# Performance work log

Hardware: AMD Instinct MI355X
Metric: run time of the kernel (lower is better)

The kernel has to match this reference:

```python
import jax, jax.numpy as jnp
import numpy as np

B, S, HID = 1, 2048, 2048
H, HKV, D = 16, 4, 128
GROUPS = H // HKV
SCALE = D ** -0.5


def rotate_half(x):
    x1, x2 = x[..., : x.shape[-1] // 2], x[..., x.shape[-1] // 2 :]
    return jnp.concatenate((-x2, x1), axis=-1)


def setup_inputs() -> dict:
    key = jax.random.key(0)
    ks = jax.random.split(key, 8)
    hidden_states = jax.random.normal(ks[0], (B, S, HID), dtype=jnp.float32)
    # standard RoPE tables, base 10000
    inv_freq = 1.0 / (10000.0 ** (np.arange(0, D, 2, dtype=np.float32) / D))
    t = np.arange(S, dtype=np.float32)
    freqs = np.outer(t, inv_freq)                      # (S, D/2)
    emb = np.concatenate([freqs, freqs], axis=-1)      # (S, D)
    cos = jnp.asarray(np.cos(emb)[None], dtype=jnp.float32)  # (1, S, D)
    sin = jnp.asarray(np.sin(emb)[None], dtype=jnp.float32)
    std = 0.02
    Wq = jax.random.normal(ks[1], (HID, H * D), dtype=jnp.float32) * std
    Wk = jax.random.normal(ks[2], (HID, HKV * D), dtype=jnp.float32) * std
    Wv = jax.random.normal(ks[3], (HID, HKV * D), dtype=jnp.float32) * std
    Wg = jax.random.normal(ks[4], (HID, HKV), dtype=jnp.float32) * std
    Wo = jax.random.normal(ks[5], (H * D, HID), dtype=jnp.float32) * std
    return {"hidden_states": hidden_states, "cos": cos, "sin": sin,
            "Wq": Wq, "Wk": Wk, "Wv": Wv, "Wg": Wg, "Wo": Wo}


def reference(hidden_states, cos, sin, Wq, Wk, Wv, Wg, Wo):
    b, s, _ = hidden_states.shape
    # projections -> (B, heads, S, D)
    q = (hidden_states @ Wq).reshape(b, s, H, D).transpose(0, 2, 1, 3)
    k = (hidden_states @ Wk).reshape(b, s, HKV, D).transpose(0, 2, 1, 3)
    v = (hidden_states @ Wv).reshape(b, s, HKV, D).transpose(0, 2, 1, 3)
    g = (hidden_states @ Wg).transpose(0, 2, 1)                 # (B, HKV, S)
    g = jax.nn.log_sigmoid(g.astype(jnp.float32))
    # RoPE
    c, sn = cos[:, None, :, :], sin[:, None, :, :]
    q = q * c + rotate_half(q) * sn
    k = k * c + rotate_half(k) * sn
    # GQA repeat kv heads
    k = jnp.repeat(k, GROUPS, axis=1)
    v = jnp.repeat(v, GROUPS, axis=1)
    g = jnp.repeat(g, GROUPS, axis=1)                           # (B, H, S)
    # gated power retention, deg=2, parallel (quadratic) form
    G = jnp.cumsum(g, axis=-1)                                  # (B, H, S)
    # decay_ij = exp(G_i - G_j) for j <= i  (<= 1 since logsigmoid < 0)
    logdecay = G[..., :, None] - G[..., None, :]                # (B, H, S, S)
    causal = jnp.tril(jnp.ones((s, s), dtype=bool))
    decay = jnp.where(causal, jnp.exp(logdecay), 0.0)
    qk = jnp.einsum("bhid,bhjd->bhij", q, k) * SCALE
    scores = (qk * qk) * decay                                  # deg=2 power scores
    den = jnp.maximum(jnp.sum(scores, axis=-1, keepdims=True), 1.0)
    out = jnp.einsum("bhij,bhjd->bhid", scores, v) / den        # (B, H, S, D)
    out = out.transpose(0, 2, 1, 3).reshape(b, s, H * D)
    return out @ Wo
```

## Files before the change

kernel.cpp:

```cpp
#include <hip/hip_runtime.h>
#include <hip/hip_bf16.h>

#define S_LEN 2048
#define HID   2048
#define NH    16
#define NKV   4
#define HD    128
#define KVD   512
#define NQKV  3072
#define SCALE2 0.0078125f
#define NCH   80

typedef __bf16 bf16;
typedef __attribute__((ext_vector_type(8))) __bf16 bf16x8;
typedef __attribute__((ext_vector_type(4))) float f32x4;

__device__ __forceinline__ void gload_lds16(const bf16* g, bf16* l) {
    __builtin_amdgcn_global_load_lds((const __attribute__((address_space(1))) void*)g,
                                     (__attribute__((address_space(3))) void*)l, 16, 0, 0);
}

__device__ __forceinline__ void transpose_tile(const float* __restrict__ W,
                                               bf16* __restrict__ Wt,
                                               int K, int N, int bx, int by,
                                               int t, float (*Ts)[65])
{
    const int kb = bx * 64, nb = by * 64;
    const int tr = t >> 6, tc = t & 63;
    #pragma unroll
    for (int p = 0; p < 16; ++p) {
        int k = p * 4 + tr;
        Ts[k][tc] = W[(size_t)(kb + k) * N + nb + tc];
    }
    __syncthreads();
    const int nr = t >> 3, kc = t & 7;
    #pragma unroll
    for (int p = 0; p < 2; ++p) {
        int n = p * 32 + nr;
        bf16x8 o;
        #pragma unroll
        for (int x = 0; x < 8; ++x) o[x] = (bf16)Ts[kc * 8 + x][n];
        *(bf16x8*)&Wt[(size_t)(nb + n) * K + kb + kc * 8] = o;
    }
}

__global__ __launch_bounds__(256) void prep_kernel(const float* __restrict__ hs,
                                                   const float* __restrict__ Wq,
                                                   const float* __restrict__ Wk,
                                                   const float* __restrict__ Wv,
                                                   const float* __restrict__ Wo,
                                                   const float* __restrict__ Wg,
                                                   bf16* __restrict__ hsb,
                                                   bf16* __restrict__ WcatT,
                                                   bf16* __restrict__ WoT,
                                                   float* __restrict__ graw,
                                                   float* __restrict__ outz)
{
    __shared__ float Ts[64][65];
    const int b = blockIdx.x, tid = threadIdx.x;

    if (b < 2048) {
        int i = (b * 256 + tid) * 8;
        const float4* qp = (const float4*)&hs[i];
        float4 a = qp[0], c = qp[1];
        bf16x8 r;
        r[0]=(bf16)a.x; r[1]=(bf16)a.y; r[2]=(bf16)a.z; r[3]=(bf16)a.w;
        r[4]=(bf16)c.x; r[5]=(bf16)c.y; r[6]=(bf16)c.z; r[7]=(bf16)c.w;
        *(bf16x8*)&hsb[i] = r;
    } else if (b < 3072) {
        int lb = b - 2048;
        transpose_tile(Wq, WcatT, HID, HID, lb >> 5, lb & 31, tid, Ts);
    } else if (b < 3328) {
        int lb = b - 3072;
        transpose_tile(Wk, WcatT + (size_t)2048 * HID, HID, KVD, lb >> 3, lb & 7, tid, Ts);
    } else if (b < 3584) {
        int lb = b - 3328;
        transpose_tile(Wv, WcatT + (size_t)2560 * HID, HID, KVD, lb >> 3, lb & 7, tid, Ts);
    } else if (b < 4608) {
        int lb = b - 3584;
        transpose_tile(Wo, WoT, HID, HID, lb >> 5, lb & 31, tid, Ts);
    } else if (b < 6656) {
        int i = ((b - 4608) * 256 + tid) * 8;
        float4 z = make_float4(0.f, 0.f, 0.f, 0.f);
        *(float4*)&outz[i] = z;
        *(float4*)&outz[i + 4] = z;
    } else {
        const int w = tid >> 6, lane = tid & 63;
        const int s = (b - 6656) * 4 + w;
        float a0 = 0.f, a1 = 0.f, a2 = 0.f, a3 = 0.f;
        for (int kk = lane; kk < HID; kk += 64) {
            float h = hs[(size_t)s * HID + kk];
            const float* wr = &Wg[kk * 4];
            a0 += h * wr[0]; a1 += h * wr[1];
            a2 += h * wr[2]; a3 += h * wr[3];
        }
        #pragma unroll
        for (int off = 32; off >= 1; off >>= 1) {
            a0 += __shfl_xor(a0, off); a1 += __shfl_xor(a1, off);
            a2 += __shfl_xor(a2, off); a3 += __shfl_xor(a3, off);
        }
        if (lane == 0) {
            float vv[4] = {a0, a1, a2, a3};
            #pragma unroll
            for (int c = 0; c < 4; ++c) {
                float x = vv[c];
                graw[c * S_LEN + s] = fminf(x, 0.f) - log1pf(expf(-fabsf(x)));
            }
        }
    }
}

__device__ __forceinline__ void gemm128_core(const bf16* __restrict__ A,
                                             const bf16* __restrict__ Bt,
                                             int K, int k0, int k1, int mb, int nb,
                                             bf16 (*As)[32], bf16 (*Bs)[32],
                                             f32x4 (*acc)[4],
                                             int w, int l16, int quad, int lane)
{
    const int m0 = (w & 1) * 64, n0 = (w >> 1) * 64;
    const int srow = lane >> 2, scol = (lane & 3) * 8;

    for (int kt = k0; kt < k1; kt += 32) {
        __syncthreads();
        gload_lds16(&A [(size_t)(mb + w * 32 +      srow) * K + kt + scol], &As[w * 32     ][0]);
        gload_lds16(&A [(size_t)(mb + w * 32 + 16 + srow) * K + kt + scol], &As[w * 32 + 16][0]);
        gload_lds16(&Bt[(size_t)(nb + w * 32 +      srow) * K + kt + scol], &Bs[w * 32     ][0]);
        gload_lds16(&Bt[(size_t)(nb + w * 32 + 16 + srow) * K + kt + scol], &Bs[w * 32 + 16][0]);
        __syncthreads();

        bf16x8 af[4], bfr[4];
        #pragma unroll
        for (int t = 0; t < 4; ++t) af[t]  = *(const bf16x8*)&As[m0 + t * 16 + l16][quad * 8];
        #pragma unroll
        for (int u = 0; u < 4; ++u) bfr[u] = *(const bf16x8*)&Bs[n0 + u * 16 + l16][quad * 8];
        #pragma unroll
        for (int t = 0; t < 4; ++t)
            #pragma unroll
            for (int u = 0; u < 4; ++u)
                acc[t][u] = __builtin_amdgcn_mfma_f32_16x16x32_bf16(af[t], bfr[u], acc[t][u], 0, 0, 0);
    }
}

__global__ __launch_bounds__(256) void gemm_qkv_kernel(const bf16* __restrict__ A,
                                                       const bf16* __restrict__ Wt,
                                                       float* __restrict__ qsl,
                                                       float* __restrict__ ksl,
                                                       float* __restrict__ vsl,
                                                       int M, int K)
{
    __shared__ __attribute__((aligned(16))) bf16 As[128][32];
    __shared__ __attribute__((aligned(16))) bf16 Bs[128][32];
    const int tid = threadIdx.x, w = tid >> 6, lane = tid & 63;
    const int l16 = lane & 15, quad = lane >> 4;
    const int mb = blockIdx.x * 128, nb = blockIdx.y * 128;
    const int m0 = (w & 1) * 64, n0 = (w >> 1) * 64;
    const int z = blockIdx.z, kh = K >> 1, k0 = z * kh;

    float* qd = qsl + (size_t)z * S_LEN * HID;
    float* kd = ksl + (size_t)z * S_LEN * KVD;
    float* vd = vsl + (size_t)z * S_LEN * KVD;

    f32x4 acc[4][4] = {};
    gemm128_core(A, Wt, K, k0, k0 + kh, mb, nb, As, Bs, acc, w, l16, quad, lane);

    #pragma unroll
    for (int t = 0; t < 4; ++t)
        #pragma unroll
        for (int u = 0; u < 4; ++u)
            #pragma unroll
            for (int r = 0; r < 4; ++r) {
                int row = mb + m0 + t * 16 + quad * 4 + r;
                int col = nb + n0 + u * 16 + l16;
                float val = acc[t][u][r];
                if (nb < 2048)       qd[(size_t)row * HID + col] = val;
                else if (nb < 2560)  kd[(size_t)row * KVD + (col - 2048)] = val;
                else                 vd[(size_t)(col - 2560) * S_LEN + row] = val;
            }
}

__global__ __launch_bounds__(256) void gemm_wo_kernel(const bf16* __restrict__ A,
                                                      const bf16* __restrict__ Bt,
                                                      float* __restrict__ C,
                                                      int M, int N, int K)
{
    __shared__ __attribute__((aligned(16))) bf16 As[128][32];
    __shared__ __attribute__((aligned(16))) bf16 Bs[128][32];
    const int tid = threadIdx.x, w = tid >> 6, lane = tid & 63;
    const int l16 = lane & 15, quad = lane >> 4;
    const int mb = blockIdx.x * 128, nb = blockIdx.y * 128;
    const int m0 = (w & 1) * 64, n0 = (w >> 1) * 64;
    const int kh = K >> 1, k0 = blockIdx.z * kh;

    f32x4 acc[4][4] = {};
    gemm128_core(A, Bt, K, k0, k0 + kh, mb, nb, As, Bs, acc, w, l16, quad, lane);

    #pragma unroll
    for (int t = 0; t < 4; ++t)
        #pragma unroll
        for (int u = 0; u < 4; ++u)
            #pragma unroll
            for (int r = 0; r < 4; ++r) {
                int row = mb + m0 + t * 16 + quad * 4 + r;
                int col = nb + n0 + u * 16 + l16;
                unsafeAtomicAdd(&C[(size_t)row * N + col], acc[t][u][r]);
            }
}

#define RQB (S_LEN * NH * 64 / 256)
#define RKB (S_LEN * NKV * 64 / 256)
#define RVB (S_LEN * KVD / 8 / 256)
__global__ __launch_bounds__(256) void rope_kernel(const float* __restrict__ qsl,
                                                   const float* __restrict__ ksl,
                                                   const float* __restrict__ vsl,
                                                   bf16* __restrict__ qb,
                                                   bf16* __restrict__ kb,
                                                   bf16* __restrict__ vT,
                                                   const float* __restrict__ cosb,
                                                   const float* __restrict__ sinb,
                                                   const float* __restrict__ graw,
                                                   float* __restrict__ G)
{
    const int blk = blockIdx.x;
    if (blk < RQB + RKB) {
        int idx = blk * 256 + threadIdx.x;
        const float* src; size_t ssz; bf16* dst; int s, rem, stride;
        if (blk < RQB) {
            src = qsl; ssz = (size_t)S_LEN * HID; dst = qb; stride = HID;
            s = idx / (NH * 64); rem = idx % (NH * 64);
        } else {
            idx -= RQB * 256;
            src = ksl; ssz = (size_t)S_LEN * KVD; dst = kb; stride = KVD;
            s = idx / (NKV * 64); rem = idx % (NKV * 64);
        }
        int h = rem >> 6, d = rem & 63;
        size_t base = (size_t)s * stride + h * 128 + d;
        float x0 = src[base]      + src[ssz + base];
        float x1 = src[base + 64] + src[ssz + base + 64];
        float c0 = cosb[s * 128 + d], c1 = cosb[s * 128 + d + 64];
        float n0 = sinb[s * 128 + d], n1 = sinb[s * 128 + d + 64];
        dst[base]      = (bf16)(x0 * c0 - x1 * n0);
        dst[base + 64] = (bf16)(x1 * c1 + x0 * n1);
    } else if (blk < RQB + RKB + RVB) {
        int i = ((blk - RQB - RKB) * 256 + threadIdx.x) * 8;
        const size_t ssz = (size_t)S_LEN * KVD;
        bf16x8 r;
        #pragma unroll
        for (int x = 0; x < 8; ++x) r[x] = (bf16)(vsl[i + x] + vsl[ssz + i + x]);
        *(bf16x8*)&vT[i] = r;
    } else {
        const int c = blk - (RQB + RKB + RVB);
        const int t = threadIdx.x;
        __shared__ float sums[256];
        float loc[8];
        float run = 0.f;
        #pragma unroll
        for (int i = 0; i < 8; ++i) { run += graw[c * S_LEN + t * 8 + i]; loc[i] = run; }
        sums[t] = run;
        __syncthreads();
        for (int off = 1; off < 256; off <<= 1) {
            float add = (t >= off) ? sums[t - off] : 0.f;
            __syncthreads();
            sums[t] += add;
            __syncthreads();
        }
        float offset = sums[t] - run;
        #pragma unroll
        for (int i = 0; i < 8; ++i) G[c * S_LEN + t * 8 + i] = offset + loc[i];
    }
}

__global__ __launch_bounds__(256) void attn_kernel(const bf16* __restrict__ q,
                                                   const bf16* __restrict__ k,
                                                   const bf16* __restrict__ vT,
                                                   const float* __restrict__ G,
                                                   bf16* __restrict__ out,
                                                   float* __restrict__ pO,
                                                   float* __restrict__ pden)
{
    int rem = blockIdx.x, qt = 0, cch = 0;
    #pragma unroll
    for (int g = 0; g < 4; ++g) {
        int sz = 8 * (g + 1);
        if (rem < sz) { qt = g * 8 + rem / (g + 1); cch = rem % (g + 1); break; }
        rem -= sz;
    }
    const int gg = qt >> 3, nc = gg + 1;
    const int jt0 = cch * 8, jt1 = min(qt + 1, jt0 + 8);

    const int h = blockIdx.y, kvh = h >> 2;
    const int qb = qt * 64;
    const int tid = threadIdx.x, w = tid >> 6, lane = tid & 63;
    const int l16 = lane & 15, quad = lane >> 4;

    __shared__ __attribute__((aligned(16))) bf16 Ks4[4][64][32];
    __shared__ __attribute__((aligned(16))) bf16 Vt4[2][128][32];
    __shared__ __attribute__((aligned(16))) bf16 Sb[4][16][68];

    bf16x8 qf[4];
    const int qrow = qb + w * 16 + l16;
    #pragma unroll
    for (int kc = 0; kc < 4; ++kc)
        qf[kc] = *(const bf16x8*)&q[(size_t)qrow * HID + h * HD + kc * 32 + quad * 8];

    const int irow = qb + w * 16 + quad * 4;
    float Gq[4];
    #pragma unroll
    for (int r = 0; r < 4; ++r) Gq[r] = G[kvh * S_LEN + irow + r];

    const int sr4 = lane >> 2, sc4 = (lane & 3) * 8;
    const int vkk = w >> 1, vdg = (w & 1) * 4;

    f32x4 acco[8] = {};
    float den[4] = {0.f, 0.f, 0.f, 0.f};

    for (int kt = jt0; kt < jt1; ++kt) {
        const int jb = kt * 64;
        __syncthreads();
        #pragma unroll
        for (int rg = 0; rg < 4; ++rg)
            gload_lds16(&k[(size_t)(jb + rg * 16 + sr4) * KVD + kvh * HD + w * 32 + sc4],
                        &Ks4[w][rg * 16][0]);
        #pragma unroll
        for (int it = 0; it < 4; ++it)
            gload_lds16(&vT[(size_t)(kvh * HD + (vdg + it) * 16 + sr4) * S_LEN + jb + vkk * 32 + sc4],
                        &Vt4[vkk][(vdg + it) * 16][0]);
        __syncthreads();

        f32x4 accs[4] = {};
        #pragma unroll
        for (int t = 0; t < 4; ++t)
            #pragma unroll
            for (int kc = 0; kc < 4; ++kc) {
                bf16x8 bfr = *(const bf16x8*)&Ks4[kc][t * 16 + l16][quad * 8];
                accs[t] = __builtin_amdgcn_mfma_f32_16x16x32_bf16(qf[kc], bfr, accs[t], 0, 0, 0);
            }

        const float Gt = G[kvh * S_LEN + jb];
        float sr[4];
        #pragma unroll
        for (int r = 0; r < 4; ++r) sr[r] = SCALE2 * __expf(Gq[r] - Gt);
        #pragma unroll
        for (int t = 0; t < 4; ++t) {
            int j = jb + t * 16 + l16;
            float colF = __expf(fminf(Gt - G[kvh * S_LEN + j], 85.f));
            #pragma unroll
            for (int r = 0; r < 4; ++r) {
                float d0 = accs[t][r];
                float sc = (j <= irow + r) ? d0 * d0 * sr[r] * colF : 0.f;
                den[r] += sc;
                Sb[w][quad * 4 + r][t * 16 + l16] = (bf16)sc;
            }
        }

        #pragma unroll
        for (int kk = 0; kk < 2; ++kk) {
            bf16x8 af = *(const bf16x8*)&Sb[w][l16][kk * 32 + quad * 8];
            #pragma unroll
            for (int dt = 0; dt < 8; ++dt) {
                bf16x8 bfr = *(const bf16x8*)&Vt4[kk][dt * 16 + l16][quad * 8];
                acco[dt] = __builtin_amdgcn_mfma_f32_16x16x32_bf16(af, bfr, acco[dt], 0, 0, 0);
            }
        }
    }

    #pragma unroll
    for (int r = 0; r < 4; ++r) {
        #pragma unroll
        for (int off = 1; off < 16; off <<= 1) den[r] += __shfl_xor(den[r], off);
    }

    if (nc == 1) {
        float dinv[4];
        #pragma unroll
        for (int r = 0; r < 4; ++r) dinv[r] = 1.f / fmaxf(den[r], 1.f);
        #pragma unroll
        for (int dt = 0; dt < 8; ++dt)
            #pragma unroll
            for (int r = 0; r < 4; ++r)
                out[(size_t)(irow + r) * HID + h * HD + dt * 16 + l16] =
                    (bf16)(acco[dt][r] * dinv[r]);
    } else {
        const int slot = h * NCH + 4 * gg * (gg + 1) + (qt & 7) * (gg + 1) + cch;
        float* po = &pO[(size_t)slot * 8192];
        const int lr = w * 16 + quad * 4;
        #pragma unroll
        for (int dt = 0; dt < 8; ++dt)
            #pragma unroll
            for (int r = 0; r < 4; ++r)
                po[(lr + r) * 128 + dt * 16 + l16] = acco[dt][r];
        if (l16 == 0) {
            #pragma unroll
            for (int r = 0; r < 4; ++r) pden[slot * 64 + lr + r] = den[r];
        }
    }
}

__global__ __launch_bounds__(256) void attn_reduce_kernel(const float* __restrict__ pO,
                                                          const float* __restrict__ pden,
                                                          bf16* __restrict__ out)
{
    const int p = blockIdx.x;
    const int h = p / 24, qt = 8 + p % 24;
    const int gg = qt >> 3, nc = gg + 1;
    const int base = h * NCH + 4 * gg * (gg + 1) + (qt & 7) * (gg + 1);
    const int qb = qt * 64;
    const int tid = threadIdx.x;

    __shared__ float sden[64];
    if (tid < 64) {
        float s = 0.f;
        for (int c = 0; c < nc; ++c) s += pden[(base + c) * 64 + tid];
        sden[tid] = 1.f / fmaxf(s, 1.f);
    }
    __syncthreads();

    #pragma unroll
    for (int i = 0; i < 8; ++i) {
        int e = i * 1024 + tid * 4;
        float4 s = make_float4(0.f, 0.f, 0.f, 0.f);
        for (int c = 0; c < nc; ++c) {
            float4 v = *(const float4*)&pO[(size_t)(base + c) * 8192 + e];
            s.x += v.x; s.y += v.y; s.z += v.z; s.w += v.w;
        }
        int lr = e >> 7, col = e & 127;
        float di = sden[lr];
        bf16* o = &out[(size_t)(qb + lr) * HID + h * HD + col];
        o[0] = (bf16)(s.x * di); o[1] = (bf16)(s.y * di);
        o[2] = (bf16)(s.z * di); o[3] = (bf16)(s.w * di);
    }
}

extern "C" void kernel_launch(void* const* d_in, const int* in_sizes, int n_in,
                              void* d_out, int out_size, void* d_ws, size_t ws_size,
                              hipStream_t stream)
{
    const float* hs   = (const float*)d_in[0];
    const float* cosb = (const float*)d_in[1];
    const float* sinb = (const float*)d_in[2];
    const float* Wq   = (const float*)d_in[3];
    const float* Wk   = (const float*)d_in[4];
    const float* Wv   = (const float*)d_in[5];
    const float* Wg   = (const float*)d_in[6];
    const float* Wo   = (const float*)d_in[7];
    float* out = (float*)d_out;

    char* p = (char*)d_ws;
    bf16*  qbuf  = (bf16*)p;  p += (size_t)S_LEN * HID * 2;
    bf16*  kbuf  = (bf16*)p;  p += (size_t)S_LEN * KVD * 2;
    bf16*  vT    = (bf16*)p;  p += (size_t)S_LEN * KVD * 2;
    bf16*  abuf  = (bf16*)p;  p += (size_t)S_LEN * HID * 2;
    bf16*  hsb   = (bf16*)p;  p += (size_t)S_LEN * HID * 2;
    bf16*  WcatT = (bf16*)p;  p += (size_t)NQKV * HID * 2;
    bf16*  WoT   = (bf16*)p;  p += (size_t)HID * HID * 2;
    float* graw  = (float*)p; p += (size_t)NKV * S_LEN * 4;
    float* G     = (float*)p; p += (size_t)NKV * S_LEN * 4;
    float* pO    = (float*)p; p += (size_t)NH * NCH * 8192 * 4;
    float* pden  = (float*)p; p += (size_t)NH * NCH * 64 * 4;

    float* qsl = pO;
    float* ksl = pO + (size_t)8 * 1024 * 1024;
    float* vsl = (float*)abuf;

    prep_kernel<<<7168, 256, 0, stream>>>(hs, Wq, Wk, Wv, Wo, Wg,
                                          hsb, WcatT, WoT, graw, out);
    gemm_qkv_kernel<<<dim3(16, 24, 2), 256, 0, stream>>>(hsb, WcatT, qsl, ksl, vsl, S_LEN, HID);
    rope_kernel<<<RQB + RKB + RVB + NKV, 256, 0, stream>>>(qsl, ksl, vsl, qbuf, kbuf, vT,
                                                           cosb, sinb, graw, G);
    attn_kernel<<<dim3(NCH, NH), 256, 0, stream>>>(qbuf, kbuf, vT, G, abuf, pO, pden);
    attn_reduce_kernel<<<NH * 24, 256, 0, stream>>>(pO, pden, abuf);
    gemm_wo_kernel<<<dim3(16, 16, 2), 256, 0, stream>>>(abuf, WoT, out, S_LEN, HID, HID);
}
```

Before: 295.7 us.

## Triple-buffer LDS tiles in projection GEMMs to overlap global loads with MFMA

Replaces the single-buffered GEMM main loop, which synchronized twice per k-tile, with a three-stage LDS ring. Tiles are prefetched two steps ahead via global_load_lds, with explicit vmcnt waits and a single barrier per iteration. The goal is to hide global-memory latency behind MFMA work in the QKV and Wo projections. In exchange, LDS use per block triples, which may reduce occupancy, and the hand-placed waitcnt and barrier ordering must stay correct.

```diff
diff --git a/kernel.cpp b/kernel.cpp
--- a/kernel.cpp
+++ b/kernel.cpp
@@ -110,35 +110,60 @@
     }
 }
 
-__device__ __forceinline__ void gemm128_core(const bf16* __restrict__ A,
+__device__ __forceinline__ void gemm128_pipe(const bf16* __restrict__ A,
                                              const bf16* __restrict__ Bt,
-                                             int K, int k0, int k1, int mb, int nb,
-                                             bf16 (*As)[32], bf16 (*Bs)[32],
+                                             int K, int k0, int nt, int mb, int nb,
+                                             bf16 (*As)[128][32], bf16 (*Bs)[128][32],
                                              f32x4 (*acc)[4],
                                              int w, int l16, int quad, int lane)
 {
     const int m0 = (w & 1) * 64, n0 = (w >> 1) * 64;
     const int srow = lane >> 2, scol = (lane & 3) * 8;
-
-    for (int kt = k0; kt < k1; kt += 32) {
-        __syncthreads();
-        gload_lds16(&A [(size_t)(mb + w * 32 +      srow) * K + kt + scol], &As[w * 32     ][0]);
-        gload_lds16(&A [(size_t)(mb + w * 32 + 16 + srow) * K + kt + scol], &As[w * 32 + 16][0]);
-        gload_lds16(&Bt[(size_t)(nb + w * 32 +      srow) * K + kt + scol], &Bs[w * 32     ][0]);
-        gload_lds16(&Bt[(size_t)(nb + w * 32 + 16 + srow) * K + kt + scol], &Bs[w * 32 + 16][0]);
-        __syncthreads();
-
+    const bf16* a0 = &A [(size_t)(mb + w * 32 +      srow) * K + k0 + scol];
+    const bf16* a1 = &A [(size_t)(mb + w * 32 + 16 + srow) * K + k0 + scol];
+    const bf16* b0 = &Bt[(size_t)(nb + w * 32 +      srow) * K + k0 + scol];
+    const bf16* b1 = &Bt[(size_t)(nb + w * 32 + 16 + srow) * K + k0 + scol];
+
+#define ISSUE_TILE(T, BUF) do {                                         \
+        gload_lds16(a0 + (size_t)(T) * 32, &As[BUF][w * 32     ][0]);   \
+        gload_lds16(a1 + (size_t)(T) * 32, &As[BUF][w * 32 + 16][0]);   \
+        gload_lds16(b0 + (size_t)(T) * 32, &Bs[BUF][w * 32     ][0]);   \
+        gload_lds16(b1 + (size_t)(T) * 32, &Bs[BUF][w * 32 + 16][0]);   \
+    } while (0)
+
+    ISSUE_TILE(0, 0);
+    ISSUE_TILE(1, 1);
+    asm volatile("s_waitcnt vmcnt(4)" ::: "memory");
+    __builtin_amdgcn_s_barrier();
+    __builtin_amdgcn_sched_barrier(0);
+
+    int cb = 0;
+    for (int t = 0; t < nt; ++t) {
         bf16x8 af[4], bfr[4];
         #pragma unroll
-        for (int t = 0; t < 4; ++t) af[t]  = *(const bf16x8*)&As[m0 + t * 16 + l16][quad * 8];
-        #pragma unroll
-        for (int u = 0; u < 4; ++u) bfr[u] = *(const bf16x8*)&Bs[n0 + u * 16 + l16][quad * 8];
-        #pragma unroll
-        for (int t = 0; t < 4; ++t)
+        for (int x = 0; x < 4; ++x) af[x]  = *(const bf16x8*)&As[cb][m0 + x * 16 + l16][quad * 8];
+        #pragma unroll
+        for (int u = 0; u < 4; ++u) bfr[u] = *(const bf16x8*)&Bs[cb][n0 + u * 16 + l16][quad * 8];
+        #pragma unroll
+        for (int x = 0; x < 4; ++x)
             #pragma unroll
             for (int u = 0; u < 4; ++u)
-                acc[t][u] = __builtin_amdgcn_mfma_f32_16x16x32_bf16(af[t], bfr[u], acc[t][u], 0, 0, 0);
-    }
+                acc[x][u] = __builtin_amdgcn_mfma_f32_16x16x32_bf16(af[x], bfr[u], acc[x][u], 0, 0, 0);
+
+        if (t + 2 < nt) {
+            const int ib = (cb == 0) ? 2 : cb - 1;
+            ISSUE_TILE(t + 2, ib);
+            asm volatile("s_waitcnt vmcnt(4)" ::: "memory");
+            __builtin_amdgcn_s_barrier();
+            __builtin_amdgcn_sched_barrier(0);
+        } else if (t + 1 < nt) {
+            asm volatile("s_waitcnt vmcnt(0)" ::: "memory");
+            __builtin_amdgcn_s_barrier();
+            __builtin_amdgcn_sched_barrier(0);
+        }
+        cb = (cb == 2) ? 0 : cb + 1;
+    }
+#undef ISSUE_TILE
 }
 
 __global__ __launch_bounds__(256) void gemm_qkv_kernel(const bf16* __restrict__ A,
@@ -148,8 +173,8 @@
                                                        float* __restrict__ vsl,
                                                        int M, int K)
 {
-    __shared__ __attribute__((aligned(16))) bf16 As[128][32];
-    __shared__ __attribute__((aligned(16))) bf16 Bs[128][32];
+    __shared__ __attribute__((aligned(16))) bf16 As[3][128][32];
+    __shared__ __attribute__((aligned(16))) bf16 Bs[3][128][32];
     const int tid = threadIdx.x, w = tid >> 6, lane = tid & 63;
     const int l16 = lane & 15, quad = lane >> 4;
     const int mb = blockIdx.x * 128, nb = blockIdx.y * 128;
@@ -161,7 +186,7 @@
     float* vd = vsl + (size_t)z * S_LEN * KVD;
 
     f32x4 acc[4][4] = {};
-    gemm128_core(A, Wt, K, k0, k0 + kh, mb, nb, As, Bs, acc, w, l16, quad, lane);
+    gemm128_pipe(A, Wt, K, k0, kh >> 5, mb, nb, As, Bs, acc, w, l16, quad, lane);
 
     #pragma unroll
     for (int t = 0; t < 4; ++t)
@@ -183,8 +208,8 @@
                                                       float* __restrict__ C,
                                                       int M, int N, int K)
 {
-    __shared__ __attribute__((aligned(16))) bf16 As[128][32];
-    __shared__ __attribute__((aligned(16))) bf16 Bs[128][32];
+    __shared__ __attribute__((aligned(16))) bf16 As[3][128][32];
+    __shared__ __attribute__((aligned(16))) bf16 Bs[3][128][32];
     const int tid = threadIdx.x, w = tid >> 6, lane = tid & 63;
     const int l16 = lane & 15, quad = lane >> 4;
     const int mb = blockIdx.x * 128, nb = blockIdx.y * 128;
@@ -192,7 +217,7 @@
     const int kh = K >> 1, k0 = blockIdx.z * kh;
 
     f32x4 acc[4][4] = {};
-    gemm128_core(A, Bt, K, k0, k0 + kh, mb, nb, As, Bs, acc, w, l16, quad, lane);
+    gemm128_pipe(A, Bt, K, k0, kh >> 5, mb, nb, As, Bs, acc, w, l16, quad, lane);
 
     #pragma unroll
     for (int t = 0; t < 4; ++t)
```

New measurement: 299.5 us. About the same (+1.3%).

## Replace 128x128 GEMM core with double-buffered 256x256 eight-phase pipelined MFMA kernel

Applied to the files above, without the earlier changes.

Swaps the simple 128x128 tile GEMM (sync, load, compute per K-step) for a 256x256 tile, 512-thread kernel with double-buffered LDS, XOR-swizzled layout, and an 8-phase schedule. Each phase interleaves global-to-LDS staging with MFMA work, using explicit vmcnt waits, barriers and setprio. It aims to hide memory latency and raise MFMA utilisation in the QKV and Wo projections. In exchange the grids get smaller (192 and 128 blocks), which may underfill the CUs, and register pressure rises from the 8x4 accumulator array.

```diff
diff --git a/kernel.cpp b/kernel.cpp
--- a/kernel.cpp
+++ b/kernel.cpp
@@ -110,99 +110,150 @@
     }
 }
 
-__device__ __forceinline__ void gemm128_core(const bf16* __restrict__ A,
-                                             const bf16* __restrict__ Bt,
-                                             int K, int k0, int k1, int mb, int nb,
-                                             bf16 (*As)[32], bf16 (*Bs)[32],
-                                             f32x4 (*acc)[4],
-                                             int w, int l16, int quad, int lane)
-{
-    const int m0 = (w & 1) * 64, n0 = (w >> 1) * 64;
-    const int srow = lane >> 2, scol = (lane & 3) * 8;
-
-    for (int kt = k0; kt < k1; kt += 32) {
-        __syncthreads();
-        gload_lds16(&A [(size_t)(mb + w * 32 +      srow) * K + kt + scol], &As[w * 32     ][0]);
-        gload_lds16(&A [(size_t)(mb + w * 32 + 16 + srow) * K + kt + scol], &As[w * 32 + 16][0]);
-        gload_lds16(&Bt[(size_t)(nb + w * 32 +      srow) * K + kt + scol], &Bs[w * 32     ][0]);
-        gload_lds16(&Bt[(size_t)(nb + w * 32 + 16 + srow) * K + kt + scol], &Bs[w * 32 + 16][0]);
-        __syncthreads();
-
-        bf16x8 af[4], bfr[4];
-        #pragma unroll
-        for (int t = 0; t < 4; ++t) af[t]  = *(const bf16x8*)&As[m0 + t * 16 + l16][quad * 8];
-        #pragma unroll
-        for (int u = 0; u < 4; ++u) bfr[u] = *(const bf16x8*)&Bs[n0 + u * 16 + l16][quad * 8];
-        #pragma unroll
-        for (int t = 0; t < 4; ++t)
-            #pragma unroll
-            for (int u = 0; u < 4; ++u)
-                acc[t][u] = __builtin_amdgcn_mfma_f32_16x16x32_bf16(af[t], bfr[u], acc[t][u], 0, 0, 0);
-    }
-}
-
-__global__ __launch_bounds__(256) void gemm_qkv_kernel(const bf16* __restrict__ A,
-                                                       const bf16* __restrict__ Wt,
-                                                       float* __restrict__ qsl,
-                                                       float* __restrict__ ksl,
-                                                       float* __restrict__ vsl,
-                                                       int M, int K)
-{
-    __shared__ __attribute__((aligned(16))) bf16 As[128][32];
-    __shared__ __attribute__((aligned(16))) bf16 Bs[128][32];
-    const int tid = threadIdx.x, w = tid >> 6, lane = tid & 63;
-    const int l16 = lane & 15, quad = lane >> 4;
-    const int mb = blockIdx.x * 128, nb = blockIdx.y * 128;
-    const int m0 = (w & 1) * 64, n0 = (w >> 1) * 64;
-    const int z = blockIdx.z, kh = K >> 1, k0 = z * kh;
+#define STG_A(G, KT, BUF) do { if ((KT) < NT)                                  \
+    gload_lds16(aS[G] + (size_t)(k0t + (KT)) * 64,                             \
+                AsL + (BUF) * 16384 + (G) * 4096 + ldst); } while (0)
+#define STG_B(G, KT, BUF) do { if ((KT) < NT)                                  \
+    gload_lds16(bS[G] + (size_t)(k0t + (KT)) * 64,                             \
+                BsL + (BUF) * 16384 + (G) * 4096 + ldst); } while (0)
+#define VMWAIT(KTN) do { if ((KTN) < NT) asm volatile("s_waitcnt vmcnt(2)" ::: "memory"); \
+                         else            asm volatile("s_waitcnt vmcnt(0)" ::: "memory"); } while (0)
+#define PH(BUF, KH, QN, STG, VM) do {                                          \
+    if ((QN) == 0) {                                                           \
+        _Pragma("unroll")                                                      \
+        for (int fm_ = 0; fm_ < 8; ++fm_)                                      \
+            af[fm_] = *(const bf16x8*)(AsL + (BUF) * 16384 +                   \
+                        (wm * 8 + fm_) * 1024 + (KH) * 512 + soR2);            \
+    }                                                                          \
+    b0 = *(const bf16x8*)(BsL + (BUF) * 16384 + (wn * 4 + 2*(QN))   * 1024 + (KH) * 512 + soR2); \
+    b1 = *(const bf16x8*)(BsL + (BUF) * 16384 + (wn * 4 + 2*(QN)+1) * 1024 + (KH) * 512 + soR2); \
+    STG;                                                                       \
+    __builtin_amdgcn_s_barrier();                                              \
+    asm volatile("s_waitcnt lgkmcnt(0)" ::: "memory");                         \
+    __builtin_amdgcn_sched_barrier(0);                                         \
+    __builtin_amdgcn_s_setprio(1);                                             \
+    _Pragma("unroll")                                                          \
+    for (int fm_ = 0; fm_ < 8; ++fm_) {                                        \
+        acc[fm_][2*(QN)]   = __builtin_amdgcn_mfma_f32_16x16x32_bf16(af[fm_], b0, acc[fm_][2*(QN)],   0, 0, 0); \
+        acc[fm_][2*(QN)+1] = __builtin_amdgcn_mfma_f32_16x16x32_bf16(af[fm_], b1, acc[fm_][2*(QN)+1], 0, 0, 0); \
+    }                                                                          \
+    __builtin_amdgcn_s_setprio(0);                                             \
+    __builtin_amdgcn_sched_barrier(0);                                         \
+    VM;                                                                        \
+    __builtin_amdgcn_s_barrier();                                              \
+} while (0)
+
+__device__ __forceinline__ void gemm256_8ph(const bf16* __restrict__ A,
+                                            const bf16* __restrict__ Bt,
+                                            int K, int k0t, int NT,
+                                            int mb, int nb,
+                                            bf16* AsL, bf16* BsL,
+                                            f32x4 (*acc)[4], int tid)
+{
+    const int l  = tid & 63;
+    const int wm = (tid >> 6) >> 2, wn = (tid >> 6) & 3;
+
+    const int so  = (tid & 63) * 16;
+    const int sos = so ^ (((so >> 9) & 1) << 5);
+    const int stg_row = ((tid >> 7) << 4) | (sos >> 6);
+    const int stg_ke  = (((((tid >> 6) & 1) << 6) | (sos & 63)) >> 1);
+    const bf16* aS[4]; const bf16* bS[4];
+    #pragma unroll
+    for (int g = 0; g < 4; ++g) {
+        aS[g] = &A [(size_t)(mb + g * 64 + stg_row) * K + stg_ke];
+        bS[g] = &Bt[(size_t)(nb + g * 64 + stg_row) * K + stg_ke];
+    }
+    const int ldst = tid * 8;
+
+    const int x    = (l & 15) * 64 + (l >> 4) * 16;
+    const int soR2 = (x ^ (((x >> 9) & 1) << 5)) >> 1;
+
+    bf16x8 af[8], b0, b1;
+
+    #pragma unroll
+    for (int g = 0; g < 4; ++g) STG_A(g, 0, 0);
+    #pragma unroll
+    for (int g = 0; g < 4; ++g) STG_B(g, 0, 0);
+    STG_A(0, 1, 1); STG_A(1, 1, 1);
+    asm volatile("s_waitcnt vmcnt(2)" ::: "memory");
+    __builtin_amdgcn_s_barrier();
+
+    const int nit = NT >> 1;
+    for (int i = 0; i < nit; ++i) {
+        const int kt1 = 2 * i + 1, kt2 = 2 * i + 2, kt3 = 2 * i + 3;
+        PH(0, 0, 0, { STG_A(2, kt1, 1); STG_A(3, kt1, 1); }, (void)0);
+        PH(0, 0, 1, { STG_B(0, kt1, 1); STG_B(1, kt1, 1); }, (void)0);
+        PH(0, 1, 0, { STG_B(2, kt1, 1); STG_B(3, kt1, 1); }, (void)0);
+        PH(0, 1, 1, { STG_A(0, kt2, 0); STG_A(1, kt2, 0); }, VMWAIT(kt2));
+        PH(1, 0, 0, { STG_A(2, kt2, 0); STG_A(3, kt2, 0); }, (void)0);
+        PH(1, 0, 1, { STG_B(0, kt2, 0); STG_B(1, kt2, 0); }, (void)0);
+        PH(1, 1, 0, { STG_B(2, kt2, 0); STG_B(3, kt2, 0); }, (void)0);
+        PH(1, 1, 1, { STG_A(0, kt3, 1); STG_A(1, kt3, 1); }, VMWAIT(kt3));
+    }
+}
+
+__global__ __launch_bounds__(512, 2) void gemm_qkv_kernel(const bf16* __restrict__ A,
+                                                          const bf16* __restrict__ Wt,
+                                                          float* __restrict__ qsl,
+                                                          float* __restrict__ ksl,
+                                                          float* __restrict__ vsl,
+                                                          int M, int K)
+{
+    __shared__ __attribute__((aligned(16))) bf16 AsL[2 * 16384];
+    __shared__ __attribute__((aligned(16))) bf16 BsL[2 * 16384];
+    const int tid = threadIdx.x;
+    const int mb = blockIdx.x * 256, nb = blockIdx.y * 256;
+    const int z = blockIdx.z, k0t = z * 16;
 
     float* qd = qsl + (size_t)z * S_LEN * HID;
     float* kd = ksl + (size_t)z * S_LEN * KVD;
     float* vd = vsl + (size_t)z * S_LEN * KVD;
 
-    f32x4 acc[4][4] = {};
-    gemm128_core(A, Wt, K, k0, k0 + kh, mb, nb, As, Bs, acc, w, l16, quad, lane);
-
-    #pragma unroll
-    for (int t = 0; t < 4; ++t)
-        #pragma unroll
-        for (int u = 0; u < 4; ++u)
+    f32x4 acc[8][4] = {};
+    gemm256_8ph(A, Wt, K, k0t, 16, mb, nb, AsL, BsL, acc, tid);
+
+    const int l16 = tid & 15, quad = (tid & 63) >> 4;
+    const int wm = (tid >> 6) >> 2, wn = (tid >> 6) & 3;
+    #pragma unroll
+    for (int fm = 0; fm < 8; ++fm)
+        #pragma unroll
+        for (int fn = 0; fn < 4; ++fn)
             #pragma unroll
             for (int r = 0; r < 4; ++r) {
-                int row = mb + m0 + t * 16 + quad * 4 + r;
-                int col = nb + n0 + u * 16 + l16;
-                float val = acc[t][u][r];
+                int row = mb + wm * 128 + fm * 16 + quad * 4 + r;
+                int col = nb + wn * 64 + fn * 16 + l16;
+                float val = acc[fm][fn][r];
                 if (nb < 2048)       qd[(size_t)row * HID + col] = val;
                 else if (nb < 2560)  kd[(size_t)row * KVD + (col - 2048)] = val;
                 else                 vd[(size_t)(col - 2560) * S_LEN + row] = val;
             }
 }
 
-__global__ __launch_bounds__(256) void gemm_wo_kernel(const bf16* __restrict__ A,
-                                                      const bf16* __restrict__ Bt,
-                                                      float* __restrict__ C,
-                                                      int M, int N, int K)
-{
-    __shared__ __attribute__((aligned(16))) bf16 As[128][32];
-    __shared__ __attribute__((aligned(16))) bf16 Bs[128][32];
-    const int tid = threadIdx.x, w = tid >> 6, lane = tid & 63;
-    const int l16 = lane & 15, quad = lane >> 4;
-    const int mb = blockIdx.x * 128, nb = blockIdx.y * 128;
-    const int m0 = (w & 1) * 64, n0 = (w >> 1) * 64;
-    const int kh = K >> 1, k0 = blockIdx.z * kh;
-
-    f32x4 acc[4][4] = {};
-    gemm128_core(A, Bt, K, k0, k0 + kh, mb, nb, As, Bs, acc, w, l16, quad, lane);
-
-    #pragma unroll
-    for (int t = 0; t < 4; ++t)
-        #pragma unroll
-        for (int u = 0; u < 4; ++u)
+__global__ __launch_bounds__(512, 2) void gemm_wo_kernel(const bf16* __restrict__ A,
+                                                         const bf16* __restrict__ Bt,
+                                                         float* __restrict__ C,
+                                                         int M, int N, int K)
+{
+    __shared__ __attribute__((aligned(16))) bf16 AsL[2 * 16384];
+    __shared__ __attribute__((aligned(16))) bf16 BsL[2 * 16384];
+    const int tid = threadIdx.x;
+    const int mb = blockIdx.x * 256, nb = blockIdx.y * 256;
+    const int k0t = blockIdx.z * 16;
+
+    f32x4 acc[8][4] = {};
+    gemm256_8ph(A, Bt, K, k0t, 16, mb, nb, AsL, BsL, acc, tid);
+
+    const int l16 = tid & 15, quad = (tid & 63) >> 4;
+    const int wm = (tid >> 6) >> 2, wn = (tid >> 6) & 3;
+    #pragma unroll
+    for (int fm = 0; fm < 8; ++fm)
+        #pragma unroll
+        for (int fn = 0; fn < 4; ++fn)
             #pragma unroll
             for (int r = 0; r < 4; ++r) {
-                int row = mb + m0 + t * 16 + quad * 4 + r;
-                int col = nb + n0 + u * 16 + l16;
-                unsafeAtomicAdd(&C[(size_t)row * N + col], acc[t][u][r]);
+                int row = mb + wm * 128 + fm * 16 + quad * 4 + r;
+                int col = nb + wn * 64 + fn * 16 + l16;
+                unsafeAtomicAdd(&C[(size_t)row * N + col], acc[fm][fn][r]);
             }
 }
 
@@ -463,10 +514,10 @@
 
     prep_kernel<<<7168, 256, 0, stream>>>(hs, Wq, Wk, Wv, Wo, Wg,
                                           hsb, WcatT, WoT, graw, out);
-    gemm_qkv_kernel<<<dim3(16, 24, 2), 256, 0, stream>>>(hsb, WcatT, qsl, ksl, vsl, S_LEN, HID);
+    gemm_qkv_kernel<<<dim3(8, 12, 2), 512, 0, stream>>>(hsb, WcatT, qsl, ksl, vsl, S_LEN, HID);
     rope_kernel<<<RQB + RKB + RVB + NKV, 256, 0, stream>>>(qsl, ksl, vsl, qbuf, kbuf, vT,
                                                            cosb, sinb, graw, G);
     attn_kernel<<<dim3(NCH, NH), 256, 0, stream>>>(qbuf, kbuf, vT, G, abuf, pO, pden);
     attn_reduce_kernel<<<NH * 24, 256, 0, stream>>>(pO, pden, abuf);
-    gemm_wo_kernel<<<dim3(16, 16, 2), 256, 0, stream>>>(abuf, WoT, out, S_LEN, HID, HID);
-}
+    gemm_wo_kernel<<<dim3(8, 8, 2), 512, 0, stream>>>(abuf, WoT, out, S_LEN, HID, HID);
+}
```

Result: slower. 308.3 us (+4.3%).

## Fuse gate projection into cast, swizzle GEMM block order, vectorize rope

Applied to the files above, without the earlier changes.

Computes the gate logsigmoid projection inside the hidden-state bf16 conversion blocks, reusing already-loaded activations and dropping the separate gate blocks. Remaps GEMM block ids so consecutive blocks on each XCD share tiles for better L2 reuse. Vectorizes RoPE and V conversion loads/stores with float4 and bf16x4. Adds a block-wide sync in the cast path.

```diff
diff --git a/kernel.cpp b/kernel.cpp
--- a/kernel.cpp
+++ b/kernel.cpp
@@ -13,6 +13,7 @@
 
 typedef __bf16 bf16;
 typedef __attribute__((ext_vector_type(8))) __bf16 bf16x8;
+typedef __attribute__((ext_vector_type(4))) __bf16 bf16x4;
 typedef __attribute__((ext_vector_type(4))) float f32x4;
 
 __device__ __forceinline__ void gload_lds16(const bf16* g, bf16* l) {
@@ -57,6 +58,7 @@
                                                    float* __restrict__ outz)
 {
     __shared__ float Ts[64][65];
+    __shared__ float red[4][4];
     const int b = blockIdx.x, tid = threadIdx.x;
 
     if (b < 2048) {
@@ -67,6 +69,33 @@
         r[0]=(bf16)a.x; r[1]=(bf16)a.y; r[2]=(bf16)a.z; r[3]=(bf16)a.w;
         r[4]=(bf16)c.x; r[5]=(bf16)c.y; r[6]=(bf16)c.z; r[7]=(bf16)c.w;
         *(bf16x8*)&hsb[i] = r;
+
+        const float4* wgp = (const float4*)&Wg[tid * 32];
+        float h[8] = {a.x, a.y, a.z, a.w, c.x, c.y, c.z, c.w};
+        float a0 = 0.f, a1 = 0.f, a2 = 0.f, a3 = 0.f;
+        #pragma unroll
+        for (int x = 0; x < 8; ++x) {
+            float4 w = wgp[x];
+            a0 += h[x] * w.x; a1 += h[x] * w.y;
+            a2 += h[x] * w.z; a3 += h[x] * w.w;
+        }
+        #pragma unroll
+        for (int off = 32; off >= 1; off >>= 1) {
+            a0 += __shfl_xor(a0, off); a1 += __shfl_xor(a1, off);
+            a2 += __shfl_xor(a2, off); a3 += __shfl_xor(a3, off);
+        }
+        const int w4 = tid >> 6;
+        if ((tid & 63) == 0) {
+            red[w4][0] = a0; red[w4][1] = a1; red[w4][2] = a2; red[w4][3] = a3;
+        }
+        __syncthreads();
+        if (tid == 0) {
+            #pragma unroll
+            for (int cc = 0; cc < 4; ++cc) {
+                float x = red[0][cc] + red[1][cc] + red[2][cc] + red[3][cc];
+                graw[cc * S_LEN + b] = fminf(x, 0.f) - log1pf(expf(-fabsf(x)));
+            }
+        }
     } else if (b < 3072) {
         int lb = b - 2048;
         transpose_tile(Wq, WcatT, HID, HID, lb >> 5, lb & 31, tid, Ts);
@@ -79,34 +108,11 @@
     } else if (b < 4608) {
         int lb = b - 3584;
         transpose_tile(Wo, WoT, HID, HID, lb >> 5, lb & 31, tid, Ts);
-    } else if (b < 6656) {
+    } else {
         int i = ((b - 4608) * 256 + tid) * 8;
         float4 z = make_float4(0.f, 0.f, 0.f, 0.f);
         *(float4*)&outz[i] = z;
         *(float4*)&outz[i + 4] = z;
-    } else {
-        const int w = tid >> 6, lane = tid & 63;
-        const int s = (b - 6656) * 4 + w;
-        float a0 = 0.f, a1 = 0.f, a2 = 0.f, a3 = 0.f;
-        for (int kk = lane; kk < HID; kk += 64) {
-            float h = hs[(size_t)s * HID + kk];
-            const float* wr = &Wg[kk * 4];
-            a0 += h * wr[0]; a1 += h * wr[1];
-            a2 += h * wr[2]; a3 += h * wr[3];
-        }
-        #pragma unroll
-        for (int off = 32; off >= 1; off >>= 1) {
-            a0 += __shfl_xor(a0, off); a1 += __shfl_xor(a1, off);
-            a2 += __shfl_xor(a2, off); a3 += __shfl_xor(a3, off);
-        }
-        if (lane == 0) {
-            float vv[4] = {a0, a1, a2, a3};
-            #pragma unroll
-            for (int c = 0; c < 4; ++c) {
-                float x = vv[c];
-                graw[c * S_LEN + s] = fminf(x, 0.f) - log1pf(expf(-fabsf(x)));
-            }
-        }
     }
 }
 
@@ -152,7 +158,11 @@
     __shared__ __attribute__((aligned(16))) bf16 Bs[128][32];
     const int tid = threadIdx.x, w = tid >> 6, lane = tid & 63;
     const int l16 = lane & 15, quad = lane >> 4;
-    const int mb = blockIdx.x * 128, nb = blockIdx.y * 128;
+
+    const int bid = blockIdx.x;
+    const int lin = (bid & 7) * 48 + (bid >> 3);
+    const int mb = (lin / 24) * 128, nb = (lin % 24) * 128;
+
     const int m0 = (w & 1) * 64, n0 = (w >> 1) * 64;
     const int z = blockIdx.z, kh = K >> 1, k0 = z * kh;
 
@@ -187,7 +197,11 @@
     __shared__ __attribute__((aligned(16))) bf16 Bs[128][32];
     const int tid = threadIdx.x, w = tid >> 6, lane = tid & 63;
     const int l16 = lane & 15, quad = lane >> 4;
-    const int mb = blockIdx.x * 128, nb = blockIdx.y * 128;
+
+    const int bid = blockIdx.x;
+    const int lin = (bid & 7) * 32 + (bid >> 3);
+    const int mb = (lin >> 4) * 128, nb = (lin & 15) * 128;
+
     const int m0 = (w & 1) * 64, n0 = (w >> 1) * 64;
     const int kh = K >> 1, k0 = blockIdx.z * kh;
 
@@ -206,9 +220,9 @@
             }
 }
 
-#define RQB (S_LEN * NH * 64 / 256)
-#define RKB (S_LEN * NKV * 64 / 256)
-#define RVB (S_LEN * KVD / 8 / 256)
+#define RQB2 2048
+#define RKB2 512
+#define RVB  512
 __global__ __launch_bounds__(256) void rope_kernel(const float* __restrict__ qsl,
                                                    const float* __restrict__ ksl,
                                                    const float* __restrict__ vsl,
@@ -221,34 +235,53 @@
                                                    float* __restrict__ G)
 {
     const int blk = blockIdx.x;
-    if (blk < RQB + RKB) {
-        int idx = blk * 256 + threadIdx.x;
+    if (blk < RQB2 + RKB2) {
+        int idx;
         const float* src; size_t ssz; bf16* dst; int s, rem, stride;
-        if (blk < RQB) {
+        if (blk < RQB2) {
+            idx = (blk * 256 + threadIdx.x) * 4;
             src = qsl; ssz = (size_t)S_LEN * HID; dst = qb; stride = HID;
             s = idx / (NH * 64); rem = idx % (NH * 64);
         } else {
-            idx -= RQB * 256;
+            idx = ((blk - RQB2) * 256 + threadIdx.x) * 4;
             src = ksl; ssz = (size_t)S_LEN * KVD; dst = kb; stride = KVD;
             s = idx / (NKV * 64); rem = idx % (NKV * 64);
         }
         int h = rem >> 6, d = rem & 63;
         size_t base = (size_t)s * stride + h * 128 + d;
-        float x0 = src[base]      + src[ssz + base];
-        float x1 = src[base + 64] + src[ssz + base + 64];
-        float c0 = cosb[s * 128 + d], c1 = cosb[s * 128 + d + 64];
-        float n0 = sinb[s * 128 + d], n1 = sinb[s * 128 + d + 64];
-        dst[base]      = (bf16)(x0 * c0 - x1 * n0);
-        dst[base + 64] = (bf16)(x1 * c1 + x0 * n1);
-    } else if (blk < RQB + RKB + RVB) {
-        int i = ((blk - RQB - RKB) * 256 + threadIdx.x) * 8;
+        float4 lo0 = *(const float4*)&src[base];
+        float4 lo1 = *(const float4*)&src[ssz + base];
+        float4 hi0 = *(const float4*)&src[base + 64];
+        float4 hi1 = *(const float4*)&src[ssz + base + 64];
+        float4 cl  = *(const float4*)&cosb[s * 128 + d];
+        float4 ch  = *(const float4*)&cosb[s * 128 + d + 64];
+        float4 sl  = *(const float4*)&sinb[s * 128 + d];
+        float4 sh  = *(const float4*)&sinb[s * 128 + d + 64];
+        float x0[4] = {lo0.x + lo1.x, lo0.y + lo1.y, lo0.z + lo1.z, lo0.w + lo1.w};
+        float x1[4] = {hi0.x + hi1.x, hi0.y + hi1.y, hi0.z + hi1.z, hi0.w + hi1.w};
+        float clo[4] = {cl.x, cl.y, cl.z, cl.w}, chi[4] = {ch.x, ch.y, ch.z, ch.w};
+        float slo[4] = {sl.x, sl.y, sl.z, sl.w}, shi[4] = {sh.x, sh.y, sh.z, sh.w};
+        bf16x4 olo, ohi;
+        #pragma unroll
+        for (int x = 0; x < 4; ++x) {
+            olo[x] = (bf16)(x0[x] * clo[x] - x1[x] * slo[x]);
+            ohi[x] = (bf16)(x1[x] * chi[x] + x0[x] * shi[x]);
+        }
+        *(bf16x4*)&dst[base]      = olo;
+        *(bf16x4*)&dst[base + 64] = ohi;
+    } else if (blk < RQB2 + RKB2 + RVB) {
+        int i = ((blk - RQB2 - RKB2) * 256 + threadIdx.x) * 8;
         const size_t ssz = (size_t)S_LEN * KVD;
+        float4 u0 = *(const float4*)&vsl[i],       u1 = *(const float4*)&vsl[i + 4];
+        float4 v0 = *(const float4*)&vsl[ssz + i], v1 = *(const float4*)&vsl[ssz + i + 4];
         bf16x8 r;
-        #pragma unroll
-        for (int x = 0; x < 8; ++x) r[x] = (bf16)(vsl[i + x] + vsl[ssz + i + x]);
+        r[0] = (bf16)(u0.x + v0.x); r[1] = (bf16)(u0.y + v0.y);
+        r[2] = (bf16)(u0.z + v0.z); r[3] = (bf16)(u0.w + v0.w);
+        r[4] = (bf16)(u1.x + v1.x); r[5] = (bf16)(u1.y + v1.y);
+        r[6] = (bf16)(u1.z + v1.z); r[7] = (bf16)(u1.w + v1.w);
         *(bf16x8*)&vT[i] = r;
     } else {
-        const int c = blk - (RQB + RKB + RVB);
+        const int c = blk - (RQB2 + RKB2 + RVB);
         const int t = threadIdx.x;
         __shared__ float sums[256];
         float loc[8];
@@ -461,12 +494,12 @@
     float* ksl = pO + (size_t)8 * 1024 * 1024;
     float* vsl = (float*)abuf;
 
-    prep_kernel<<<7168, 256, 0, stream>>>(hs, Wq, Wk, Wv, Wo, Wg,
+    prep_kernel<<<6656, 256, 0, stream>>>(hs, Wq, Wk, Wv, Wo, Wg,
                                           hsb, WcatT, WoT, graw, out);
-    gemm_qkv_kernel<<<dim3(16, 24, 2), 256, 0, stream>>>(hsb, WcatT, qsl, ksl, vsl, S_LEN, HID);
-    rope_kernel<<<RQB + RKB + RVB + NKV, 256, 0, stream>>>(qsl, ksl, vsl, qbuf, kbuf, vT,
-                                                           cosb, sinb, graw, G);
+    gemm_qkv_kernel<<<dim3(384, 1, 2), 256, 0, stream>>>(hsb, WcatT, qsl, ksl, vsl, S_LEN, HID);
+    rope_kernel<<<RQB2 + RKB2 + RVB + NKV, 256, 0, stream>>>(qsl, ksl, vsl, qbuf, kbuf, vT,
+                                                             cosb, sinb, graw, G);
     attn_kernel<<<dim3(NCH, NH), 256, 0, stream>>>(qbuf, kbuf, vT, G, abuf, pO, pden);
     attn_reduce_kernel<<<NH * 24, 256, 0, stream>>>(pO, pden, abuf);
-    gemm_wo_kernel<<<dim3(16, 16, 2), 256, 0, stream>>>(abuf, WoT, out, S_LEN, HID, HID);
-}
+    gemm_wo_kernel<<<dim3(256, 1, 2), 256, 0, stream>>>(abuf, WoT, out, S_LEN, HID, HID);
+}
```

New measurement: 281.6 us. 1.05x faster.
